# Optimization experiments

Measured on AMD Instinct MI355X. Metric: run time of the kernel, lower is better.

The kernel has to match this reference:

```python
import jax, jax.numpy as jnp
import numpy as np

B, TM, SM, V = 16, 128, 64, 1024
NEG = jnp.float32(-1e30)  # safe stand-in for -inf (avoids nan in grads)


def setup_inputs() -> dict:
    key = jax.random.key(0)
    k1, k2 = jax.random.split(key)
    acts = jax.random.normal(k1, (B * TM * (SM + 1), V), dtype=jnp.float32)
    labels = jax.random.randint(k2, (B, SM), 1, V, dtype=jnp.int32)
    input_lengths = jnp.full((B,), TM, dtype=jnp.int32)
    label_lengths = jnp.full((B,), SM, dtype=jnp.int32)
    return {"acts": acts, "labels": labels, "input_lengths": input_lengths,
            "label_lengths": label_lengths, "T_max": TM, "S_max": SM}


def _monotonic_rnnt_loss(acts, labels, input_lengths, label_lengths, T_max, S_max, blank=0):
    """Monotonic RNN-T: each time frame emits exactly one symbol (blank keeps
    label position, a label advances it). Loss = -log p(labels | acts).
    acts is packed row-major: row(b,t,s) = off_b + t*(S_b+1) + s."""
    Bq = labels.shape[0]
    N = acts.shape[0]
    T = input_lengths.astype(jnp.int32)
    S = label_lengths.astype(jnp.int32)
    Sp1 = S + 1
    sizes = T * Sp1
    off = jnp.concatenate([jnp.zeros((1,), jnp.int32), jnp.cumsum(sizes)[:-1]])

    # log-softmax normalizer per packed row (softmax done internally by the loss)
    lse = jax.scipy.special.logsumexp(acts, axis=1)  # [N]

    t_idx = jnp.arange(T_max)[None, :, None]          # [1,T,1]
    s_idx = jnp.arange(S_max + 1)[None, None, :]      # [1,1,S+1]
    rows = off[:, None, None] + t_idx * Sp1[:, None, None] + s_idx  # [B,T,S+1]
    rows_c = jnp.clip(rows, 0, N - 1)

    valid_b = (t_idx < T[:, None, None]) & (s_idx <= S[:, None, None])
    blank_lp = jnp.where(valid_b, acts[rows_c, blank] - lse[rows_c], NEG)  # [B,T,S+1]

    lab_rows = rows_c[:, :, :S_max]                   # [B,T,S]
    valid_l = (t_idx < T[:, None, None]) & (s_idx[:, :, :S_max] < S[:, None, None])
    # gather log p(y_{s+1} | b, t, s) without materializing [B,T,S,V]
    label_lp = jnp.where(valid_l,
                         acts[lab_rows, labels[:, None, :]] - lse[lab_rows], NEG)  # [B,T,S]

    blank_t = jnp.transpose(blank_lp, (1, 0, 2))  # [T,B,S+1]
    label_t = jnp.transpose(label_lp, (1, 0, 2))  # [T,B,S]

    alpha0 = jnp.full((Bq, S_max + 1), NEG, dtype=acts.dtype).at[:, 0].set(0.0)

    def step(alpha, inp):
        t, blp, llp = inp
        # stay (blank) or advance one label
        shifted = jnp.concatenate(
            [jnp.full((Bq, 1), NEG, dtype=acts.dtype), alpha[:, :-1] + llp], axis=1)
        new = jnp.logaddexp(alpha + blp, shifted)
        # freeze alpha past each sequence's last frame
        return jnp.where(t < T[:, None], new, alpha), None

    alpha, _ = jax.lax.scan(step, alpha0, (jnp.arange(T_max), blank_t, label_t))
    return -alpha[jnp.arange(Bq), S]


def reference(acts, labels, input_lengths, label_lengths, T_max, S_max):
    return _monotonic_rnnt_loss(acts, labels, input_lengths, label_lengths, T_max, S_max, blank=0)
```

## Files before the change

kernel.cpp:

```cpp
#include <hip/hip_runtime.h>
#include <math.h>

#define Bc 16
#define TM 128
#define SMAX 64
#define VV 1024
#define NEGF (-1e30f)

typedef float f32x4 __attribute__((ext_vector_type(4)));

__device__ __forceinline__ float wave_sum64(float v) {
  for (int o = 32; o > 0; o >>= 1) v += __shfl_down(v, o);
  return __shfl(v, 0);
}
__device__ __forceinline__ float logaddexp_f(float a, float b) {
  float m = fmaxf(a, b);
  float d = fminf(a, b) - m;
  return m + __logf(1.0f + __expf(d));
}

__device__ __forceinline__ float sum16exp(f32x4 a, f32x4 b, f32x4 c, f32x4 d) {
  return __expf(a.x) + __expf(a.y) + __expf(a.z) + __expf(a.w) +
         __expf(b.x) + __expf(b.y) + __expf(b.z) + __expf(b.w) +
         __expf(c.x) + __expf(c.y) + __expf(c.z) + __expf(c.w) +
         __expf(d.x) + __expf(d.y) + __expf(d.z) + __expf(d.w);
}

__global__ __launch_bounds__(256) void rnnt_lp_kernel(
    const float* __restrict__ acts, const int* __restrict__ labels,
    const int* __restrict__ Tlen, const int* __restrict__ Slen,
    float* __restrict__ blank_lp, float* __restrict__ label_lp)
{
  const int lane = threadIdx.x & 63;
  const int wv   = threadIdx.x >> 6;
  const int cell0 = blockIdx.x * 8 + wv * 2;
  const int total = Bc * TM * (SMAX + 1);

  long long row[2];
  int bb[2], tt[2], ss[2], Sb_[2];
  bool valid[2];
  #pragma unroll
  for (int k = 0; k < 2; ++k) {
    const int cell = cell0 + k;
    const int b   = cell / (TM * (SMAX + 1));
    const int rem = cell % (TM * (SMAX + 1));
    const int t = rem / (SMAX + 1);
    const int s = rem % (SMAX + 1);
    bb[k] = b; tt[k] = t; ss[k] = s;
    const int Tb = Tlen[b], Sb = Slen[b];
    Sb_[k] = Sb;
    valid[k] = (cell < total) && (t < Tb) && (s <= Sb);
    long long off = 0;
    for (int i = 0; i < b; ++i) off += (long long)Tlen[i] * (Slen[i] + 1);
    row[k] = off + (long long)t * (Sb + 1) + s;
  }

  f32x4 x[2][4];
  #pragma unroll
  for (int k = 0; k < 2; ++k) {
    if (valid[k]) {
      const f32x4* rp = (const f32x4*)(acts + row[k] * (long long)VV);
      x[k][0] = __builtin_nontemporal_load(rp + lane);
      x[k][1] = __builtin_nontemporal_load(rp + lane + 64);
      x[k][2] = __builtin_nontemporal_load(rp + lane + 128);
      x[k][3] = __builtin_nontemporal_load(rp + lane + 192);
    }
  }

  #pragma unroll
  for (int k = 0; k < 2; ++k) {
    const int cell = cell0 + k;
    if (cell >= total) continue;
    const int b = bb[k], t = tt[k], s = ss[k], Sb = Sb_[k];
    const int lab_idx = (b * TM + t) * SMAX + s;

    if (!valid[k]) {
      if (lane == 0) {
        blank_lp[cell] = NEGF;
        if (s < SMAX) label_lp[lab_idx] = NEGF;
      }
      continue;
    }

    float ssum = sum16exp(x[k][0], x[k][1], x[k][2], x[k][3]);
    ssum = wave_sum64(ssum);
    const float lse = __logf(ssum);

    if (lane == 0) blank_lp[cell] = x[k][0].x - lse;

    if (s < Sb) {
      const int lab  = labels[b * SMAX + s];
      const int f    = lab >> 2;
      const int comp = lab & 3;
      const int src  = f & 63;
      const int j    = f >> 6;
      f32x4 xx = (j == 0) ? x[k][0] : (j == 1) ? x[k][1] : (j == 2) ? x[k][2] : x[k][3];
      float v = (comp == 0) ? xx.x : (comp == 1) ? xx.y : (comp == 2) ? xx.z : xx.w;
      v = __shfl(v, src);
      if (lane == 0) label_lp[lab_idx] = v - lse;
    } else if (s < SMAX) {
      if (lane == 0) label_lp[lab_idx] = NEGF;
    }
  }
}

__global__ __launch_bounds__(64) void rnnt_alpha_kernel(
    const float* __restrict__ blank_lp, const float* __restrict__ label_lp,
    const int* __restrict__ Tlen, const int* __restrict__ Slen,
    float* __restrict__ out)
{
  __shared__ __align__(16) float sb[TM * (SMAX + 1)];
  __shared__ __align__(16) float sl[TM * SMAX];
  const int b = blockIdx.x;
  const int lane = threadIdx.x;

  const float* gb = blank_lp + (size_t)b * TM * (SMAX + 1);
  const float* gl = label_lp + (size_t)b * TM * SMAX;
  for (int i = lane * 4; i < TM * (SMAX + 1); i += 64 * 4)
    *(float4*)&sb[i] = *(const float4*)&gb[i];
  for (int i = lane * 4; i < TM * SMAX; i += 64 * 4)
    *(float4*)&sl[i] = *(const float4*)&gl[i];
  __syncthreads();

  const int Tb = Tlen[b], Sb = Slen[b];
  float a    = (lane == 0) ? 0.0f : NEGF;
  float a_hi = NEGF;

  for (int t = 0; t < Tb; ++t) {
    const float blp      = sb[t * (SMAX + 1) + lane];
    const float llp_prev = (lane >= 1) ? sl[t * SMAX + lane - 1] : NEGF;
    const float blp64    = sb[t * (SMAX + 1) + 64];
    const float llp63    = sl[t * SMAX + 63];
    const float a_prev   = __shfl_up(a, 1);
    const float a63      = __shfl(a, 63);
    const float newv = logaddexp_f(a + blp,
                                   (lane >= 1) ? (a_prev + llp_prev) : NEGF);
    const float new_hi = logaddexp_f(a_hi + blp64, a63 + llp63);
    a = newv;
    a_hi = new_hi;
  }

  const float via_shfl = __shfl(a, Sb & 63);
  const float aS = (Sb < 64) ? via_shfl : a_hi;
  if (lane == 0) out[b] = -aS;
}

extern "C" void kernel_launch(void* const* d_in, const int* in_sizes, int n_in,
                              void* d_out, int out_size, void* d_ws, size_t ws_size,
                              hipStream_t stream) {
  const float* acts  = (const float*)d_in[0];
  const int* labels  = (const int*)d_in[1];
  const int* Tlen    = (const int*)d_in[2];
  const int* Slen    = (const int*)d_in[3];
  float* out = (float*)d_out;

  float* blank_lp = (float*)d_ws;
  float* label_lp = blank_lp + Bc * TM * (SMAX + 1);

  const int cells = Bc * TM * (SMAX + 1);
  rnnt_lp_kernel<<<(cells + 7) / 8, 256, 0, stream>>>(
      acts, labels, Tlen, Slen, blank_lp, label_lp);
  rnnt_alpha_kernel<<<Bc, 64, 0, stream>>>(
      blank_lp, label_lp, Tlen, Slen, out);
}
```

Before: 698.3 us.

## Process 16 rows per wave with double-buffered loads and wave-level prefix offsets

Each wave now handles 16 consecutive cells and prefetches the next pair of rows while computing on the current pair, so memory latency can overlap with the exp/reduce work. Per-batch offsets come from a one-time wave prefix scan rather than a serial loop over earlier batches for every cell. Nontemporal loads are replaced with ordinary loads, and the alpha kernel uses 256 threads to stage its shared memory faster. In exchange, register pressure rises and there are fewer waves in flight, which the launch bound of 4 blocks tries to control.

```diff
diff --git a/kernel.cpp b/kernel.cpp
--- a/kernel.cpp
+++ b/kernel.cpp
@@ -6,10 +6,12 @@
 #define SMAX 64
 #define VV 1024
 #define NEGF (-1e30f)
+#define CELLS (Bc * TM * (SMAX + 1))
 
 typedef float f32x4 __attribute__((ext_vector_type(4)));
 
 __device__ __forceinline__ float wave_sum64(float v) {
+  #pragma unroll
   for (int o = 32; o > 0; o >>= 1) v += __shfl_down(v, o);
   return __shfl(v, 0);
 }
@@ -19,92 +21,116 @@
   return m + __logf(1.0f + __expf(d));
 }
 
-__device__ __forceinline__ float sum16exp(f32x4 a, f32x4 b, f32x4 c, f32x4 d) {
-  return __expf(a.x) + __expf(a.y) + __expf(a.z) + __expf(a.w) +
-         __expf(b.x) + __expf(b.y) + __expf(b.z) + __expf(b.w) +
-         __expf(c.x) + __expf(c.y) + __expf(c.z) + __expf(c.w) +
-         __expf(d.x) + __expf(d.y) + __expf(d.z) + __expf(d.w);
-}
+#define RPW 16
+#define NPAIR (RPW / 2)
 
-__global__ __launch_bounds__(256) void rnnt_lp_kernel(
+__global__ __launch_bounds__(256, 4) void rnnt_lp_kernel(
     const float* __restrict__ acts, const int* __restrict__ labels,
     const int* __restrict__ Tlen, const int* __restrict__ Slen,
     float* __restrict__ blank_lp, float* __restrict__ label_lp)
 {
   const int lane = threadIdx.x & 63;
   const int wv   = threadIdx.x >> 6;
-  const int cell0 = blockIdx.x * 8 + wv * 2;
-  const int total = Bc * TM * (SMAX + 1);
+  const int wave = blockIdx.x * 4 + wv;
+  const int cbase = wave * RPW;
+  if (cbase >= CELLS) return;
 
-  long long row[2];
-  int bb[2], tt[2], ss[2], Sb_[2];
-  bool valid[2];
+  const int bidx = lane & 15;
+  const int Tb_l = Tlen[bidx];
+  const int Sb_l = Slen[bidx];
+  const int sz   = Tb_l * (Sb_l + 1);
+  int incl = sz;
   #pragma unroll
-  for (int k = 0; k < 2; ++k) {
-    const int cell = cell0 + k;
+  for (int o = 1; o < 16; o <<= 1) {
+    int u = __shfl_up(incl, o);
+    if (bidx >= o) incl += u;
+  }
+  const int excl = incl - sz;
+
+  struct Geo {
+    int lab_idx;
+    int s, Sb, lab;
+    long long row;
+    bool val;
+  };
+
+  auto geo = [&](int cell) {
+    Geo g;
     const int b   = cell / (TM * (SMAX + 1));
-    const int rem = cell % (TM * (SMAX + 1));
-    const int t = rem / (SMAX + 1);
-    const int s = rem % (SMAX + 1);
-    bb[k] = b; tt[k] = t; ss[k] = s;
-    const int Tb = Tlen[b], Sb = Slen[b];
-    Sb_[k] = Sb;
-    valid[k] = (cell < total) && (t < Tb) && (s <= Sb);
-    long long off = 0;
-    for (int i = 0; i < b; ++i) off += (long long)Tlen[i] * (Slen[i] + 1);
-    row[k] = off + (long long)t * (Sb + 1) + s;
-  }
+    const int rem = cell - b * (TM * (SMAX + 1));
+    const int t   = rem / (SMAX + 1);
+    g.s = rem - t * (SMAX + 1);
+    const int Tb = __shfl(Tb_l, b);
+    g.Sb = __shfl(Sb_l, b);
+    const int off = __shfl(excl, b);
+    g.row = (long long)off + (long long)t * (g.Sb + 1) + g.s;
+    g.val = (t < Tb) && (g.s <= g.Sb);
+    g.lab_idx = (b * TM + t) * SMAX + g.s;
+    g.lab = (g.val && g.s < g.Sb) ? labels[b * SMAX + g.s] : -1;
+    return g;
+  };
 
-  f32x4 x[2][4];
-  #pragma unroll
-  for (int k = 0; k < 2; ++k) {
-    if (valid[k]) {
-      const f32x4* rp = (const f32x4*)(acts + row[k] * (long long)VV);
-      x[k][0] = __builtin_nontemporal_load(rp + lane);
-      x[k][1] = __builtin_nontemporal_load(rp + lane + 64);
-      x[k][2] = __builtin_nontemporal_load(rp + lane + 128);
-      x[k][3] = __builtin_nontemporal_load(rp + lane + 192);
+  auto issue = [&](const Geo& g, f32x4* x) {
+    if (g.val) {
+      const f32x4* rp = (const f32x4*)(acts + g.row * (long long)VV) + lane;
+      x[0] = rp[0];
+      x[1] = rp[64];
+      x[2] = rp[128];
+      x[3] = rp[192];
     }
-  }
+  };
+
+  auto compute = [&](int cell, const Geo& g, const f32x4* x) {
+    if (!g.val) {
+      if (lane == 0) {
+        blank_lp[cell] = NEGF;
+        if (g.s < SMAX) label_lp[g.lab_idx] = NEGF;
+      }
+      return;
+    }
+    float p = 0.0f;
+    #pragma unroll
+    for (int q = 0; q < 4; ++q)
+      p += __expf(x[q].x) + __expf(x[q].y) + __expf(x[q].z) + __expf(x[q].w);
+    const float lse = __logf(wave_sum64(p));
+    if (g.s < g.Sb) {
+      const int f    = g.lab >> 2;
+      const int comp = g.lab & 3;
+      const int src  = f & 63;
+      const int j    = f >> 6;
+      f32x4 xx = (j == 0) ? x[0] : (j == 1) ? x[1] : (j == 2) ? x[2] : x[3];
+      float v = (comp == 0) ? xx.x : (comp == 1) ? xx.y : (comp == 2) ? xx.z : xx.w;
+      v = __shfl(v, src);
+      if (lane == 0) label_lp[g.lab_idx] = v - lse;
+    } else if (g.s < SMAX) {
+      if (lane == 0) label_lp[g.lab_idx] = NEGF;
+    }
+    if (lane == 0) blank_lp[cell] = x[0].x - lse;
+  };
+
+  f32x4 xb[2][2][4];
+  Geo   gb[2][2];
+
+  gb[0][0] = geo(cbase + 0);
+  gb[0][1] = geo(cbase + 1);
+  issue(gb[0][0], xb[0][0]);
+  issue(gb[0][1], xb[0][1]);
 
   #pragma unroll
-  for (int k = 0; k < 2; ++k) {
-    const int cell = cell0 + k;
-    if (cell >= total) continue;
-    const int b = bb[k], t = tt[k], s = ss[k], Sb = Sb_[k];
-    const int lab_idx = (b * TM + t) * SMAX + s;
-
-    if (!valid[k]) {
-      if (lane == 0) {
-        blank_lp[cell] = NEGF;
-        if (s < SMAX) label_lp[lab_idx] = NEGF;
-      }
-      continue;
+  for (int i = 0; i < NPAIR; ++i) {
+    const int cur = i & 1, nxt = cur ^ 1;
+    if (i + 1 < NPAIR) {
+      gb[nxt][0] = geo(cbase + 2 * i + 2);
+      gb[nxt][1] = geo(cbase + 2 * i + 3);
+      issue(gb[nxt][0], xb[nxt][0]);
+      issue(gb[nxt][1], xb[nxt][1]);
     }
-
-    float ssum = sum16exp(x[k][0], x[k][1], x[k][2], x[k][3]);
-    ssum = wave_sum64(ssum);
-    const float lse = __logf(ssum);
-
-    if (lane == 0) blank_lp[cell] = x[k][0].x - lse;
-
-    if (s < Sb) {
-      const int lab  = labels[b * SMAX + s];
-      const int f    = lab >> 2;
-      const int comp = lab & 3;
-      const int src  = f & 63;
-      const int j    = f >> 6;
-      f32x4 xx = (j == 0) ? x[k][0] : (j == 1) ? x[k][1] : (j == 2) ? x[k][2] : x[k][3];
-      float v = (comp == 0) ? xx.x : (comp == 1) ? xx.y : (comp == 2) ? xx.z : xx.w;
-      v = __shfl(v, src);
-      if (lane == 0) label_lp[lab_idx] = v - lse;
-    } else if (s < SMAX) {
-      if (lane == 0) label_lp[lab_idx] = NEGF;
-    }
+    compute(cbase + 2 * i + 0, gb[cur][0], xb[cur][0]);
+    compute(cbase + 2 * i + 1, gb[cur][1], xb[cur][1]);
   }
 }
 
-__global__ __launch_bounds__(64) void rnnt_alpha_kernel(
+__global__ __launch_bounds__(256) void rnnt_alpha_kernel(
     const float* __restrict__ blank_lp, const float* __restrict__ label_lp,
     const int* __restrict__ Tlen, const int* __restrict__ Slen,
     float* __restrict__ out)
@@ -112,16 +138,18 @@
   __shared__ __align__(16) float sb[TM * (SMAX + 1)];
   __shared__ __align__(16) float sl[TM * SMAX];
   const int b = blockIdx.x;
-  const int lane = threadIdx.x;
+  const int tid = threadIdx.x;
 
   const float* gb = blank_lp + (size_t)b * TM * (SMAX + 1);
   const float* gl = label_lp + (size_t)b * TM * SMAX;
-  for (int i = lane * 4; i < TM * (SMAX + 1); i += 64 * 4)
+  for (int i = tid * 4; i < TM * (SMAX + 1); i += 256 * 4)
     *(float4*)&sb[i] = *(const float4*)&gb[i];
-  for (int i = lane * 4; i < TM * SMAX; i += 64 * 4)
+  for (int i = tid * 4; i < TM * SMAX; i += 256 * 4)
     *(float4*)&sl[i] = *(const float4*)&gl[i];
   __syncthreads();
+  if (tid >= 64) return;
 
+  const int lane = tid;
   const int Tb = Tlen[b], Sb = Slen[b];
   float a    = (lane == 0) ? 0.0f : NEGF;
   float a_hi = NEGF;
@@ -157,9 +185,10 @@
   float* blank_lp = (float*)d_ws;
   float* label_lp = blank_lp + Bc * TM * (SMAX + 1);
 
-  const int cells = Bc * TM * (SMAX + 1);
-  rnnt_lp_kernel<<<(cells + 7) / 8, 256, 0, stream>>>(
+  const int waves_total  = (CELLS + RPW - 1) / RPW;
+  const int blocks       = (waves_total + 3) / 4;
+  rnnt_lp_kernel<<<blocks, 256, 0, stream>>>(
       acts, labels, Tlen, Slen, blank_lp, label_lp);
-  rnnt_alpha_kernel<<<Bc, 64, 0, stream>>>(
+  rnnt_alpha_kernel<<<Bc, 256, 0, stream>>>(
       blank_lp, label_lp, Tlen, Slen, out);
 }
```

New measurement: 726.0 us. 4.0% more time.
